# Performance work log

Hardware: AMD Instinct MI355X
Metric: run time of the kernel (lower is better)

## Reference

```python
import jax, jax.numpy as jnp
import numpy as np

IGNORE_INDEX = -100
B, S, D, V = 4, 2048, 2048, 32000


def setup_inputs() -> dict:
    key = jax.random.key(0)
    k1, k2, k3, k4 = jax.random.split(key, 4)
    hidden = jax.random.normal(k1, (B, S, D), dtype=jnp.float32)
    targets = jax.random.randint(k2, (B, S), 0, V, dtype=jnp.int64)
    drop = jax.random.uniform(k3, (B, S)) < 0.1
    targets = jnp.where(drop, IGNORE_INDEX, targets)
    W = jax.random.normal(k4, (V, D), dtype=jnp.float32) * (D ** -0.5)
    return {"hidden": hidden, "targets": targets, "W": W}


def reference(hidden, targets, W):
    # hidden: [B, S, D], targets: [B, S] int, W: [V, D]
    mask = targets != IGNORE_INDEX                      # [B, S]
    total = mask.sum()
    # Linear projection to vocab, CE computed in fp32 (matches logits.float())
    logits = jnp.einsum('bsd,vd->bsv', hidden, W).astype(jnp.float32)  # [B, S, V]
    logp = jax.nn.log_softmax(logits, axis=-1)
    safe_t = jnp.where(mask, targets, 0)
    nll = -jnp.take_along_axis(logp, safe_t[..., None], axis=-1)[..., 0]  # [B, S]
    loss_sum = jnp.sum(jnp.where(mask, nll, 0.0))
    return loss_sum / total.astype(jnp.float32)
```

## Files before the change

kernel.cpp:

```cpp
#include <hip/hip_runtime.h>
#include <hip/hip_bf16.h>
#include <stdint.h>

#define IGNORE_INDEX (-100)

constexpr int M_ = 8192;
constexpr int K_ = 2048;
constexpr int N_ = 32000;

constexpr int BM = 128, BN = 128;

typedef __attribute__((ext_vector_type(4)))  float f32x4;
typedef __attribute__((ext_vector_type(16))) float f32x16;
typedef __attribute__((ext_vector_type(4)))  int   i32x4;
typedef __attribute__((ext_vector_type(8)))  int   i32x8;
typedef __attribute__((ext_vector_type(4)))  unsigned int u32x4;
typedef __attribute__((ext_vector_type(8)))  __bf16 bf16x8;

#define SCALE_A 8.0f
#define SCALE_W 1024.0f
#define INV_S   (1.0f / (8.0f * 1024.0f))

__device__ __forceinline__ unsigned pack_bf16(float f0, float f1) {
    unsigned u0 = __builtin_bit_cast(unsigned, f0) + 0x8000u;
    unsigned u1 = __builtin_bit_cast(unsigned, f1) + 0x8000u;
    return __builtin_amdgcn_perm(u1, u0, 0x07060302u);
}
__device__ __forceinline__ u32x4 pack8(f32x4 lo, f32x4 hi) {
    u32x4 r;
    r[0] = pack_bf16(lo[0], lo[1]);
    r[1] = pack_bf16(lo[2], lo[3]);
    r[2] = pack_bf16(hi[0], hi[1]);
    r[3] = pack_bf16(hi[2], hi[3]);
    return r;
}

__device__ __forceinline__ void gll16(const void* g, void* l) {
    __builtin_amdgcn_global_load_lds(
        (const __attribute__((address_space(1))) unsigned int*)g,
        (__attribute__((address_space(3))) unsigned int*)l, 16, 0, 0);
}

__global__ void init_acc(float* p, int n) {
    int i = blockIdx.x * 256 + threadIdx.x;
    if (i < n) p[i] = 0.0f;
}

__global__ __launch_bounds__(256) void convert_fp8(
    const float* __restrict__ in, unsigned int* __restrict__ out,
    float scale, int n8)
{
    int i = blockIdx.x * 256 + threadIdx.x;
    if (i < n8) {
        f32x4 lo = ((const f32x4*)in)[2 * i];
        f32x4 hi = ((const f32x4*)in)[2 * i + 1];
        int w0 = 0, w1 = 0;
        w0 = __builtin_amdgcn_cvt_pk_fp8_f32(lo[0] * scale, lo[1] * scale, w0, false);
        w0 = __builtin_amdgcn_cvt_pk_fp8_f32(lo[2] * scale, lo[3] * scale, w0, true);
        w1 = __builtin_amdgcn_cvt_pk_fp8_f32(hi[0] * scale, hi[1] * scale, w1, false);
        w1 = __builtin_amdgcn_cvt_pk_fp8_f32(hi[2] * scale, hi[3] * scale, w1, true);
        out[2 * i]     = (unsigned int)w0;
        out[2 * i + 1] = (unsigned int)w1;
    }
}


#define MFMA_SC(a, b, c) \
    __builtin_amdgcn_mfma_scale_f32_32x32x64_f8f6f4( \
        (a), (b), (c), 0, 0, 0, 0x7F7F7F7F, 0, 0x7F7F7F7F)

#define STAGE(asb, bsb, koff)                          \
    do {                                               \
        gll16(gA0 + (koff), (asb) + stoff);            \
        gll16(gA1 + (koff), (asb) + stoff + 4096);     \
        gll16(gB0 + (koff), (bsb) + stoff);            \
        gll16(gB1 + (koff), (bsb) + stoff + 4096);     \
    } while (0)

#define COMPUTE(asb, bsb)                                                     \
    do {                                                                      \
        const unsigned char* pA_ = (asb);                                     \
        const unsigned char* pB_ = (bsb);                                     \
        i32x4 aL0 = *(const i32x4*)(pA_ + aoffL);                             \
        i32x4 aH0 = *(const i32x4*)(pA_ + aoffH);                             \
        i32x4 aL1 = *(const i32x4*)(pA_ + aoffL + 2048);                      \
        i32x4 aH1 = *(const i32x4*)(pA_ + aoffH + 2048);                      \
        i32x4 bL0 = *(const i32x4*)(pB_ + boffL);                             \
        i32x4 bH0 = *(const i32x4*)(pB_ + boffH);                             \
        i32x4 bL1 = *(const i32x4*)(pB_ + boffL + 2048);                      \
        i32x4 bH1 = *(const i32x4*)(pB_ + boffH + 2048);                      \
        i32x8 af0 = (i32x8){aL0[0], aL0[1], aL0[2], aL0[3],                   \
                            aH0[0], aH0[1], aH0[2], aH0[3]};                  \
        i32x8 af1 = (i32x8){aL1[0], aL1[1], aL1[2], aL1[3],                   \
                            aH1[0], aH1[1], aH1[2], aH1[3]};                  \
        i32x8 bf0 = (i32x8){bL0[0], bL0[1], bL0[2], bL0[3],                   \
                            bH0[0], bH0[1], bH0[2], bH0[3]};                  \
        i32x8 bf1 = (i32x8){bL1[0], bL1[1], bL1[2], bL1[3],                   \
                            bH1[0], bH1[1], bH1[2], bH1[3]};                  \
        __builtin_amdgcn_s_setprio(1);                                        \
        acc00 = MFMA_SC(af0, bf0, acc00);                                     \
        acc01 = MFMA_SC(af0, bf1, acc01);                                     \
        acc10 = MFMA_SC(af1, bf0, acc10);                                     \
        acc11 = MFMA_SC(af1, bf1, acc11);                                     \
        __builtin_amdgcn_s_setprio(0);                                        \
    } while (0)

__global__ __launch_bounds__(256, 3) void gemm_fp8(
    const unsigned char* __restrict__ A,
    const unsigned char* __restrict__ Wq,
    const int*   __restrict__ tgt,
    float* __restrict__ sumexp,
    float* __restrict__ tgtlogit)
{
    __shared__ __align__(16) unsigned char As[2][BM * 64];
    __shared__ __align__(16) unsigned char Bs[2][BN * 64];
    __shared__ int tg[BM];

    const int tid = threadIdx.x;
    const int mt  = blockIdx.x;
    const int nt  = blockIdx.y;

    if (tid < BM) tg[tid] = tgt[mt * BM + tid];

    const int wave = tid >> 6;
    const int lane = tid & 63;
    const int wm   = wave >> 1;
    const int wn   = wave & 1;

    const int srow = tid >> 2;
    const int spg  = (tid & 3) ^ ((srow >> 1) & 3);
    const unsigned char* gA0 = A  + (size_t)(mt * BM + srow) * K_ + spg * 16;
    const unsigned char* gB0 = Wq + (size_t)(nt * BN + srow) * K_ + spg * 16;
    const unsigned char* gA1 = gA0 + (size_t)64 * K_;
    const unsigned char* gB1 = gB0 + (size_t)64 * K_;
    const int stoff = wave * 1024;

    const int l31 = lane & 31;
    const int h   = lane >> 5;
    const int ra  = wm * 64 + l31;
    const int rb  = wn * 64 + l31;
    const int xa  = (ra >> 1) & 3;
    const int xb  = (rb >> 1) & 3;
    const int aoffL = ra * 64 + ((2 * h)     ^ xa) * 16;
    const int aoffH = ra * 64 + ((2 * h + 1) ^ xa) * 16;
    const int boffL = rb * 64 + ((2 * h)     ^ xb) * 16;
    const int boffH = rb * 64 + ((2 * h + 1) ^ xb) * 16;

    f32x16 acc00, acc01, acc10, acc11;
#pragma unroll
    for (int r = 0; r < 16; r++) {
        acc00[r] = 0.f; acc01[r] = 0.f; acc10[r] = 0.f; acc11[r] = 0.f;
    }

    STAGE(As[0], Bs[0], 0);
    __syncthreads();

#pragma unroll 1
    for (int kt = 0; kt < K_; kt += 128) {
        STAGE(As[1], Bs[1], kt + 64);
        __builtin_amdgcn_sched_barrier(0);
        COMPUTE(As[0], Bs[0]);
        __syncthreads();

        if (kt + 128 < K_) STAGE(As[0], Bs[0], kt + 128);
        __builtin_amdgcn_sched_barrier(0);
        COMPUTE(As[1], Bs[1]);
        __syncthreads();
    }

    const int c0 = nt * BN + wn * 64 + l31;
#pragma unroll
    for (int reg = 0; reg < 16; reg++) {
        const int rbase = (reg & 3) + 8 * (reg >> 2) + 4 * h;
        {
            const int lrow = wm * 64 + rbase;
            const int grow = mt * BM + lrow;
            const int t    = tg[lrow];
            float v0 = acc00[reg] * INV_S;
            float v1 = acc01[reg] * INV_S;
            if (t == c0)      tgtlogit[grow] = v0;
            if (t == c0 + 32) tgtlogit[grow] = v1;
            float rs = __expf(v0) + __expf(v1);
            rs += __shfl_xor(rs, 1);
            rs += __shfl_xor(rs, 2);
            rs += __shfl_xor(rs, 4);
            rs += __shfl_xor(rs, 8);
            rs += __shfl_xor(rs, 16);
            if (l31 == 0) atomicAdd(&sumexp[grow], rs);
        }
        {
            const int lrow = wm * 64 + 32 + rbase;
            const int grow = mt * BM + lrow;
            const int t    = tg[lrow];
            float v0 = acc10[reg] * INV_S;
            float v1 = acc11[reg] * INV_S;
            if (t == c0)      tgtlogit[grow] = v0;
            if (t == c0 + 32) tgtlogit[grow] = v1;
            float rs = __expf(v0) + __expf(v1);
            rs += __shfl_xor(rs, 1);
            rs += __shfl_xor(rs, 2);
            rs += __shfl_xor(rs, 4);
            rs += __shfl_xor(rs, 8);
            rs += __shfl_xor(rs, 16);
            if (l31 == 0) atomicAdd(&sumexp[grow], rs);
        }
    }
}

constexpr int BKf = 32;
constexpr int LDA = BKf + 8;
__global__ __launch_bounds__(256) void gemm_fused_f32(
    const float* __restrict__ A,
    const float* __restrict__ W,
    const int*   __restrict__ tgt,
    float* __restrict__ sumexp,
    float* __restrict__ tgtlogit)
{
    __shared__ __bf16 As[BM * LDA];
    __shared__ __bf16 Bs[BN * LDA];
    __shared__ int    tg[BM];

    const int tid = threadIdx.x;
    const int mt  = blockIdx.x;
    const int nt  = blockIdx.y;
    if (tid < BM) tg[tid] = tgt[mt * BM + tid];

    const int wave = tid >> 6, lane = tid & 63;
    const int wm = wave >> 1, wn = wave & 1;
    const int lquad = lane >> 4, lcol = lane & 15;
    const int srow = tid >> 2, scol = (tid & 3) * 8;

    const float* gA = A + (size_t)(mt * BM + srow) * K_ + scol;
    const float* gB = W + (size_t)(nt * BN + srow) * K_ + scol;
    const size_t rowstep = (size_t)64 * K_;

    f32x4 acc[4][4];
#pragma unroll
    for (int i = 0; i < 4; i++)
#pragma unroll
        for (int j = 0; j < 4; j++) acc[i][j] = (f32x4){0.f, 0.f, 0.f, 0.f};

    for (int kt = 0; kt < K_; kt += BKf) {
        f32x4 a0 = *(const f32x4*)(gA + kt);
        f32x4 a1 = *(const f32x4*)(gA + kt + 4);
        f32x4 a2 = *(const f32x4*)(gA + kt + rowstep);
        f32x4 a3 = *(const f32x4*)(gA + kt + rowstep + 4);
        f32x4 b0 = *(const f32x4*)(gB + kt);
        f32x4 b1 = *(const f32x4*)(gB + kt + 4);
        f32x4 b2 = *(const f32x4*)(gB + kt + rowstep);
        f32x4 b3 = *(const f32x4*)(gB + kt + rowstep + 4);
        __syncthreads();
        *(u32x4*)&As[srow * LDA + scol]        = pack8(a0, a1);
        *(u32x4*)&As[(srow + 64) * LDA + scol] = pack8(a2, a3);
        *(u32x4*)&Bs[srow * LDA + scol]        = pack8(b0, b1);
        *(u32x4*)&Bs[(srow + 64) * LDA + scol] = pack8(b2, b3);
        __syncthreads();
        bf16x8 af[4], bf[4];
#pragma unroll
        for (int f = 0; f < 4; f++) {
            af[f] = *(const bf16x8*)&As[(wm * 64 + f * 16 + lcol) * LDA + lquad * 8];
            bf[f] = *(const bf16x8*)&Bs[(wn * 64 + f * 16 + lcol) * LDA + lquad * 8];
        }
#pragma unroll
        for (int mf = 0; mf < 4; mf++)
#pragma unroll
            for (int nf = 0; nf < 4; nf++)
                acc[mf][nf] = __builtin_amdgcn_mfma_f32_16x16x32_bf16(af[mf], bf[nf], acc[mf][nf], 0, 0, 0);
    }
    const int colbase = nt * BN + wn * 64;
#pragma unroll
    for (int mf = 0; mf < 4; mf++) {
#pragma unroll
        for (int r = 0; r < 4; r++) {
            const int lrow = wm * 64 + mf * 16 + lquad * 4 + r;
            const int grow = mt * BM + lrow;
            const int t    = tg[lrow];
            float rs = 0.f;
#pragma unroll
            for (int nf = 0; nf < 4; nf++) {
                float v = acc[mf][nf][r];
                rs += __expf(v);
                if (t == colbase + nf * 16 + lcol) tgtlogit[grow] = v;
            }
            rs += __shfl_xor(rs, 1);
            rs += __shfl_xor(rs, 2);
            rs += __shfl_xor(rs, 4);
            rs += __shfl_xor(rs, 8);
            if (lcol == 0) atomicAdd(&sumexp[grow], rs);
        }
    }
}

__global__ __launch_bounds__(256) void finalize(
    const float* __restrict__ sumexp,
    const float* __restrict__ tgtlogit,
    const int*   __restrict__ tgt,
    float* __restrict__ out)
{
    float s = 0.f;
    int   c = 0;
    for (int i = threadIdx.x; i < M_; i += 256) {
        int t = tgt[i];
        if (t != IGNORE_INDEX) {
            s += __logf(sumexp[i]) - tgtlogit[i];
            c++;
        }
    }
#pragma unroll
    for (int o = 32; o; o >>= 1) {
        s += __shfl_down(s, o);
        c += __shfl_down(c, o);
    }
    __shared__ float ss[4];
    __shared__ int   cc[4];
    int w = threadIdx.x >> 6;
    if ((threadIdx.x & 63) == 0) { ss[w] = s; cc[w] = c; }
    __syncthreads();
    if (threadIdx.x == 0) {
        float st = ss[0] + ss[1] + ss[2] + ss[3];
        int   ct = cc[0] + cc[1] + cc[2] + cc[3];
        out[0] = st / (float)ct;
    }
}

extern "C" void kernel_launch(void* const* d_in, const int* in_sizes, int n_in,
                              void* d_out, int out_size, void* d_ws, size_t ws_size,
                              hipStream_t stream) {
    const float* hidden  = (const float*)d_in[0];
    const int*   targets = (const int*)d_in[1];
    const float* W       = (const float*)d_in[2];

    float* sumexp   = (float*)d_ws;
    float* tgtlogit = sumexp + M_;
    float* out      = (float*)d_out;

    unsigned char* Aq = (unsigned char*)d_ws + 2 * M_ * sizeof(float);
    unsigned char* Wq = Aq + (size_t)M_ * K_;
    const size_t need = 2 * M_ * sizeof(float) + (size_t)M_ * K_ + (size_t)N_ * K_;

    init_acc<<<(2 * M_ + 255) / 256, 256, 0, stream>>>(sumexp, 2 * M_);

    if (ws_size >= need) {
        const int a8 = M_ * K_ / 8;
        const int w8 = N_ * K_ / 8;
        convert_fp8<<<(a8 + 255) / 256, 256, 0, stream>>>(hidden, (unsigned int*)Aq, SCALE_A, a8);
        convert_fp8<<<(w8 + 255) / 256, 256, 0, stream>>>(W, (unsigned int*)Wq, SCALE_W, w8);
        gemm_fp8<<<dim3(M_ / BM, N_ / BN), 256, 0, stream>>>(Aq, Wq, targets, sumexp, tgtlogit);
    } else {
        gemm_fused_f32<<<dim3(M_ / BM, N_ / BN), 256, 0, stream>>>(hidden, W, targets, sumexp, tgtlogit);
    }

    finalize<<<1, 256, 0, stream>>>(sumexp, tgtlogit, targets, out);
}
```

Measured before the change: 1.082 ms.

## Triple-buffer fp8 GEMM main loop with explicit vmcnt waits and single barriers

Replaces the double-buffered K loop, which had two full __syncthreads per pair of stages, with a three-stage LDS ring. The loop is unrolled by three, waits with s_waitcnt vmcnt(4) plus a raw s_barrier, and issues the next global-to-LDS load before computing the current stage. This gives loads two stages of lead time and removes the extra barrier drains. An explicit lgkmcnt(0) wait is inserted before the MFMAs. The LDS footprint grows by half, which may pressure occupancy at 3 blocks per CU.

Result: slower. 1.125 ms (+4.0%).

```diff
diff --git a/kernel.cpp b/kernel.cpp
--- a/kernel.cpp
+++ b/kernel.cpp
@@ -69,6 +69,17 @@
     __builtin_amdgcn_mfma_scale_f32_32x32x64_f8f6f4( \
         (a), (b), (c), 0, 0, 0, 0x7F7F7F7F, 0, 0x7F7F7F7F)
 
+#define LGKM0() do { \
+    asm volatile("s_waitcnt lgkmcnt(0)" ::: "memory"); \
+    __builtin_amdgcn_sched_barrier(0); \
+} while (0)
+
+#define WAITBAR(N) do { \
+    asm volatile("s_waitcnt vmcnt(" #N ")" ::: "memory"); \
+    __builtin_amdgcn_s_barrier(); \
+    __builtin_amdgcn_sched_barrier(0); \
+} while (0)
+
 #define STAGE(asb, bsb, koff)                          \
     do {                                               \
         gll16(gA0 + (koff), (asb) + stoff);            \
@@ -89,6 +100,7 @@
         i32x4 bH0 = *(const i32x4*)(pB_ + boffH);                             \
         i32x4 bL1 = *(const i32x4*)(pB_ + boffL + 2048);                      \
         i32x4 bH1 = *(const i32x4*)(pB_ + boffH + 2048);                      \
+        LGKM0();                                                              \
         i32x8 af0 = (i32x8){aL0[0], aL0[1], aL0[2], aL0[3],                   \
                             aH0[0], aH0[1], aH0[2], aH0[3]};                  \
         i32x8 af1 = (i32x8){aL1[0], aL1[1], aL1[2], aL1[3],                   \
@@ -112,8 +124,8 @@
     float* __restrict__ sumexp,
     float* __restrict__ tgtlogit)
 {
-    __shared__ __align__(16) unsigned char As[2][BM * 64];
-    __shared__ __align__(16) unsigned char Bs[2][BN * 64];
+    __shared__ __align__(16) unsigned char As[3][BM * 64];
+    __shared__ __align__(16) unsigned char Bs[3][BN * 64];
     __shared__ int tg[BM];
 
     const int tid = threadIdx.x;
@@ -153,20 +165,29 @@
     }
 
     STAGE(As[0], Bs[0], 0);
-    __syncthreads();
+    STAGE(As[1], Bs[1], 64);
+    asm volatile("s_waitcnt lgkmcnt(0)" ::: "memory");
 
 #pragma unroll 1
-    for (int kt = 0; kt < K_; kt += 128) {
-        STAGE(As[1], Bs[1], kt + 64);
-        __builtin_amdgcn_sched_barrier(0);
+    for (int it = 0; it < 10; ++it) {
+        WAITBAR(4);
+        STAGE(As[2], Bs[2], 128);
         COMPUTE(As[0], Bs[0]);
-        __syncthreads();
-
-        if (kt + 128 < K_) STAGE(As[0], Bs[0], kt + 128);
-        __builtin_amdgcn_sched_barrier(0);
+
+        WAITBAR(4);
+        STAGE(As[0], Bs[0], 192);
         COMPUTE(As[1], Bs[1]);
-        __syncthreads();
-    }
+
+        WAITBAR(4);
+        STAGE(As[1], Bs[1], 256);
+        COMPUTE(As[2], Bs[2]);
+
+        gA0 += 192; gA1 += 192; gB0 += 192; gB1 += 192;
+    }
+    WAITBAR(4);
+    COMPUTE(As[0], Bs[0]);
+    WAITBAR(0);
+    COMPUTE(As[1], Bs[1]);
 
     const int c0 = nt * BN + wn * 64 + l31;
 #pragma unroll
```
